# Optimization experiments

Hardware: AMD Instinct MI355X
Metric: run time of the kernel (lower is better)

The kernel has to match this reference:

```python
import jax, jax.numpy as jnp
import numpy as np

B, T, C = 2, 2048, 1024
NH = 16
HD = C // NH

def setup_inputs() -> dict:
    key = jax.random.key(0)
    ks = jax.random.split(key, 4)
    x = jax.random.normal(ks[0], (B, T, C), dtype=jnp.float32)
    w_attn = jax.random.normal(ks[1], (C, 3 * C), dtype=jnp.float32) * (1.0 / np.sqrt(C))
    b_attn = jnp.zeros((3 * C,), dtype=jnp.float32)
    w_proj = jax.random.normal(ks[2], (C, C), dtype=jnp.float32) * (1.0 / np.sqrt(C))
    b_proj = jnp.zeros((C,), dtype=jnp.float32)
    return {"x": x, "w_attn": w_attn, "b_attn": b_attn, "w_proj": w_proj, "b_proj": b_proj}

def reference(x, w_attn, b_attn, w_proj, b_proj):
    Bq, Tq, Cq = x.shape
    qkv = x @ w_attn + b_attn                      # [B,T,3C]
    q, k, v = jnp.split(qkv, 3, axis=2)
    # [B,T,C] -> [B,NH,T,HD]
    def heads(t):
        return t.reshape(Bq, Tq, NH, HD).transpose(0, 2, 1, 3)
    q, k, v = heads(q), heads(k), heads(v)
    att = jnp.einsum('bhqd,bhkd->bhqk', q, k) * (1.0 / np.sqrt(HD))
    causal = jnp.tril(jnp.ones((Tq, Tq), dtype=bool))
    att = jnp.where(causal[None, None], att, -jnp.inf)
    att = jax.nn.softmax(att, axis=-1)
    y = jnp.einsum('bhqk,bhkd->bhqd', att, v)      # [B,NH,T,HD]
    y = y.transpose(0, 2, 1, 3).reshape(Bq, Tq, Cq)
    return y @ w_proj + b_proj
```

## Files before the change

kernel.cpp:

```cpp
#include <hip/hip_runtime.h>

typedef unsigned short u16;
typedef short bf16x8 __attribute__((ext_vector_type(8)));
typedef float f32x4 __attribute__((ext_vector_type(4)));

#define BATCH 2
#define SEQ   2048
#define CH    1024
#define NHEAD 16
#define HDIM  64
#define ROWS  (BATCH*SEQ)

#define SWZ(r_, c_) (((r_)*64) + ((c_) ^ (((r_)&7)*8)))

__device__ __forceinline__ u16 f2b(float f) {
  unsigned u = __builtin_bit_cast(unsigned, f);
  u += 0x7FFFu + ((u >> 16) & 1u);
  return (u16)(u >> 16);
}
__device__ __forceinline__ float b2f(u16 h) {
  unsigned u = ((unsigned)h) << 16;
  return __builtin_bit_cast(float, u);
}
__device__ __forceinline__ float exp2_fast(float x) {
  float r; asm("v_exp_f32 %0, %1" : "=v"(r) : "v"(x)); return r;
}
__device__ __forceinline__ unsigned cvt_pk_bf16(float a, float b) {
  unsigned r; asm("v_cvt_pk_bf16_f32 %0, %1, %2" : "=v"(r) : "v"(a), "v"(b)); return r;
}

__device__ __forceinline__ void gload_lds16(const void* g, void* l) {
  __builtin_amdgcn_global_load_lds(
      (const __attribute__((address_space(1))) unsigned int*)g,
      (__attribute__((address_space(3))) unsigned int*)l, 16, 0, 0);
}

__global__ void csa_convert_x(const float* __restrict__ in, u16* __restrict__ out,
                              int n8) {
  int i = blockIdx.x * 256 + threadIdx.x;
  if (i >= n8) return;
  const float4* f4 = (const float4*)in;
  float4 v0 = f4[2*i], v1 = f4[2*i+1];
  ushort4 o0, o1;
  o0.x = f2b(v0.x); o0.y = f2b(v0.y); o0.z = f2b(v0.z); o0.w = f2b(v0.w);
  o1.x = f2b(v1.x); o1.y = f2b(v1.y); o1.z = f2b(v1.z); o1.w = f2b(v1.w);
  ((ushort4*)out)[2*i]   = o0;
  ((ushort4*)out)[2*i+1] = o1;
}

__global__ void csa_transpose2(const float* __restrict__ wa, const float* __restrict__ wp,
                               u16* __restrict__ wat, u16* __restrict__ wpt) {
  __shared__ float tile[32][33];
  int bx = blockIdx.x;
  const float* in; u16* out; int C;
  if (bx < 96) { in = wa; out = wat; C = 3*CH; }
  else         { in = wp; out = wpt; C = CH; bx -= 96; }
  const int R = CH;
  const int bxc = bx * 32, by = blockIdx.y * 32;
  const int tx = threadIdx.x, ty = threadIdx.y;
  #pragma unroll
  for (int j = 0; j < 4; ++j) {
    int r = by + ty + j*8, c = bxc + tx;
    tile[ty + j*8][tx] = in[(size_t)r*C + c];
  }
  __syncthreads();
  #pragma unroll
  for (int j = 0; j < 4; ++j) {
    int oc = bxc + ty + j*8;
    int orr = by + tx;
    out[(size_t)oc*R + orr] = f2b(tile[tx][ty + j*8]);
  }
}

__global__ __launch_bounds__(512) void csa_gemm_qkv(
    const u16* __restrict__ A, const u16* __restrict__ Bt,
    const float* __restrict__ bias,
    u16* __restrict__ qbo, u16* __restrict__ kb, u16* __restrict__ vtb)
{
  __shared__ __align__(16) u16 As[2][256*64];
  __shared__ __align__(16) u16 Bs[2][192*64];
  const int t = threadIdx.x, lane = t & 63, w = t >> 6;
  const int wm = w >> 2, wn = w & 3, g = lane >> 4, qi = lane & 15;

  const int wgid = blockIdx.y * 16 + blockIdx.x;
  const int c8 = wgid & 7, inner = wgid >> 3;
  const int bm = (c8 >> 1) * 4 + (inner >> 3);
  const int bn = (c8 & 1) * 8 + (inner & 7);

  f32x4 acc[8][3] = {};

  const u16* Ab = A  + (size_t)(bm*256)*CH;
  const u16* Bb = Bt + (size_t)(bn*192)*CH;
  const int srow = t >> 3;
  const int scol = (t & 7) * 8;

  #pragma unroll
  for (int p = 0; p < 4; ++p)
    gload_lds16(Ab + (size_t)(p*64 + srow)*CH + scol, &As[0][p*4096 + w*512]);
  #pragma unroll
  for (int p = 0; p < 3; ++p)
    gload_lds16(Bb + (size_t)(p*64 + srow)*CH + scol, &Bs[0][p*4096 + w*512]);
  __syncthreads();

  int cur = 0;
  for (int k0 = 0; k0 < CH; k0 += 64) {
    if (k0 + 64 < CH) {
      #pragma unroll
      for (int p = 0; p < 4; ++p)
        gload_lds16(Ab + (size_t)(p*64 + srow)*CH + (k0+64) + scol, &As[cur^1][p*4096 + w*512]);
      #pragma unroll
      for (int p = 0; p < 3; ++p)
        gload_lds16(Bb + (size_t)(p*64 + srow)*CH + (k0+64) + scol, &Bs[cur^1][p*4096 + w*512]);
    }
    #pragma unroll
    for (int kk = 0; kk < 2; ++kk) {
      bf16x8 af[8], bfr[3];
      #pragma unroll
      for (int m = 0; m < 8; ++m)
        af[m] = *(const bf16x8*)&As[cur][(wm*128 + m*16 + qi)*64 + kk*32 + g*8];
      #pragma unroll
      for (int n = 0; n < 3; ++n)
        bfr[n] = *(const bf16x8*)&Bs[cur][(wn*48 + n*16 + qi)*64 + kk*32 + g*8];
      #pragma unroll
      for (int m = 0; m < 8; ++m)
        #pragma unroll
        for (int n = 0; n < 3; ++n)
          acc[m][n] = __builtin_amdgcn_mfma_f32_16x16x32_bf16(af[m], bfr[n], acc[m][n], 0, 0, 0);
    }
    __syncthreads();
    cur ^= 1;
  }

  #pragma unroll
  for (int m = 0; m < 8; ++m) {
    const int row0 = bm*256 + wm*128 + m*16 + g*4;
    const int bb = row0 >> 11;
    const int t0 = row0 & 2047;
    #pragma unroll
    for (int n = 0; n < 3; ++n) {
      const int col = bn*192 + wn*48 + n*16 + qi;
      const float bv = bias[col];
      const int which = col >> 10;
      const int cc = col & 1023;
      const int h = cc >> 6, d = cc & 63;
      const int bh = bb*16 + h;
      if (which == 2) {
        ushort4 pw;
        pw.x = f2b(acc[m][n][0] + bv);
        pw.y = f2b(acc[m][n][1] + bv);
        pw.z = f2b(acc[m][n][2] + bv);
        pw.w = f2b(acc[m][n][3] + bv);
        *(ushort4*)&vtb[((size_t)bh*HDIM + d)*SEQ + t0] = pw;
      } else {
        u16* dst = (which == 0) ? qbo : kb;
        #pragma unroll
        for (int r = 0; r < 4; ++r)
          dst[((size_t)bh*SEQ + t0 + r)*HDIM + d] = f2b(acc[m][n][r] + bv);
      }
    }
  }
}

__global__ __launch_bounds__(256) void csa_gemm_proj(
    const u16* __restrict__ A, const u16* __restrict__ Bt,
    const float* __restrict__ bias, float* __restrict__ out)
{
  __shared__ __align__(16) u16 As[2][128*64];
  __shared__ __align__(16) u16 Bs[2][128*64];
  const int t = threadIdx.x, lane = t & 63, w = t >> 6;
  const int wm = w >> 1, wn = w & 1, g = lane >> 4, qi = lane & 15;
  const int bm = blockIdx.y, bn = blockIdx.x;

  f32x4 acc[4][4] = {};

  const u16* Ab = A  + (size_t)(bm*128)*CH;
  const u16* Bb = Bt + (size_t)(bn*128)*CH;
  const int srow = t >> 3;
  const int scol = (t & 7) * 8;

  #pragma unroll
  for (int p = 0; p < 4; ++p) {
    gload_lds16(Ab + (size_t)(p*32 + srow)*CH + scol, &As[0][p*2048 + w*512]);
    gload_lds16(Bb + (size_t)(p*32 + srow)*CH + scol, &Bs[0][p*2048 + w*512]);
  }
  __syncthreads();

  int cur = 0;
  for (int k0 = 0; k0 < CH; k0 += 64) {
    if (k0 + 64 < CH) {
      #pragma unroll
      for (int p = 0; p < 4; ++p) {
        gload_lds16(Ab + (size_t)(p*32 + srow)*CH + (k0+64) + scol, &As[cur^1][p*2048 + w*512]);
        gload_lds16(Bb + (size_t)(p*32 + srow)*CH + (k0+64) + scol, &Bs[cur^1][p*2048 + w*512]);
      }
    }
    #pragma unroll
    for (int kk = 0; kk < 2; ++kk) {
      bf16x8 af[4], bfr[4];
      #pragma unroll
      for (int m = 0; m < 4; ++m)
        af[m] = *(const bf16x8*)&As[cur][(wm*64 + m*16 + qi)*64 + kk*32 + g*8];
      #pragma unroll
      for (int n = 0; n < 4; ++n)
        bfr[n] = *(const bf16x8*)&Bs[cur][(wn*64 + n*16 + qi)*64 + kk*32 + g*8];
      #pragma unroll
      for (int m = 0; m < 4; ++m)
        #pragma unroll
        for (int n = 0; n < 4; ++n)
          acc[m][n] = __builtin_amdgcn_mfma_f32_16x16x32_bf16(af[m], bfr[n], acc[m][n], 0, 0, 0);
    }
    __syncthreads();
    cur ^= 1;
  }

  #pragma unroll
  for (int m = 0; m < 4; ++m) {
    const int row0 = bm*128 + wm*64 + m*16 + g*4;
    #pragma unroll
    for (int n = 0; n < 4; ++n) {
      const int col = bn*128 + wn*64 + n*16 + qi;
      const float bv = bias[col];
      #pragma unroll
      for (int r = 0; r < 4; ++r)
        out[(size_t)(row0 + r)*CH + col] = acc[m][n][r] + bv;
    }
  }
}

__global__ __launch_bounds__(512) void csa_attn(
    const u16* __restrict__ qb, const u16* __restrict__ kb,
    const u16* __restrict__ vtb, u16* __restrict__ yout)
{
  const int bh = blockIdx.x, pair = blockIdx.y;
  const int bidx = bh >> 4, h = bh & 15;
  const int t = threadIdx.x, lane = t & 63, w = t >> 6;
  const int g = lane >> 4, qi = lane & 15;
  __shared__ __align__(16) u16 Ks[2][64*64];
  __shared__ __align__(16) u16 Vs[2][64*64];
  __shared__ __align__(16) u16 Ps[8][16*64];

  const size_t kvbase = (size_t)bh * SEQ * HDIM;
  const int srow = t >> 3;
  const int ssw  = (srow & 7) * 8;
  const int scol = ((t & 7) * 8) ^ ssw;

  int offK[2][4], offPw[4], offPr[2];
  #pragma unroll
  for (int c = 0; c < 2; ++c) {
    offPr[c] = SWZ(qi, c*32 + g*8);
    #pragma unroll
    for (int s4 = 0; s4 < 4; ++s4) offK[c][s4] = SWZ(s4*16 + qi, c*32 + g*8);
  }
  #pragma unroll
  for (int s4 = 0; s4 < 4; ++s4) offPw[s4] = SWZ(qi, s4*16 + g*4);

  const float QSCALE = 0.18033688011112042f;

  for (int half = 0; half < 2; ++half) {
    const int qt = half ? (15 - pair) : pair;
    const int qrow = qt*128 + w*16;
    const int nkt = 2*qt + 2;
    const int kend = qrow >> 6;

    bf16x8 qf[2];
    #pragma unroll
    for (int c = 0; c < 2; ++c) {
      qf[c] = *(const bf16x8*)&qb[(kvbase + (size_t)(qrow + qi)*HDIM) + c*32 + g*8];
      #pragma unroll
      for (int e = 0; e < 8; ++e)
        qf[c][e] = (short)f2b(b2f((u16)qf[c][e]) * QSCALE);
    }

    f32x4 yacc[4] = {};
    float mrun = -1e30f, srun = 0.f;

    gload_lds16(kb  + kvbase + (size_t)srow*HDIM + scol, &Ks[0][w*512]);
    gload_lds16(vtb + kvbase + (size_t)srow*SEQ  + scol, &Vs[0][w*512]);
    __syncthreads();

    int cur = 0;
    for (int kt = 0; kt < nkt; ++kt) {
      if (kt + 1 < nkt) {
        const int k1 = (kt + 1) * 64;
        gload_lds16(kb  + kvbase + (size_t)(k1 + srow)*HDIM + scol, &Ks[cur^1][w*512]);
        gload_lds16(vtb + kvbase + (size_t)srow*SEQ + k1 + scol,    &Vs[cur^1][w*512]);
      }

      if (kt <= kend) {
        f32x4 st[4] = {};
        #pragma unroll
        for (int c = 0; c < 2; ++c)
          #pragma unroll
          for (int s4 = 0; s4 < 4; ++s4) {
            bf16x8 kf = *(const bf16x8*)&Ks[cur][offK[c][s4]];
            st[s4] = __builtin_amdgcn_mfma_f32_16x16x32_bf16(kf, qf[c], st[s4], 0, 0, 0);
          }

        if (kt == kend) {
          const int lq = (qrow & 63) + qi;
          #pragma unroll
          for (int s4 = 0; s4 < 4; ++s4)
            #pragma unroll
            for (int r = 0; r < 4; ++r)
              if (s4*16 + g*4 + r > lq) st[s4][r] = -3.0e38f;
        }

        float tmax = st[0][0];
        #pragma unroll
        for (int s4 = 0; s4 < 4; ++s4)
          #pragma unroll
          for (int r = 0; r < 4; ++r) tmax = fmaxf(tmax, st[s4][r]);
        tmax = fmaxf(tmax, __shfl_xor(tmax, 16));
        tmax = fmaxf(tmax, __shfl_xor(tmax, 32));
        if (!__all(tmax - mrun <= 11.5f)) {
          float mnew = fmaxf(mrun, tmax);
          float fac = exp2_fast(mrun - mnew);
          #pragma unroll
          for (int r = 0; r < 4; ++r) {
            float fr = __shfl(fac, g*4 + r);
            #pragma unroll
            for (int nf = 0; nf < 4; ++nf) yacc[nf][r] *= fr;
          }
          srun *= fac;
          mrun = mnew;
        }
        float tsum = 0.f;
        #pragma unroll
        for (int s4 = 0; s4 < 4; ++s4)
          #pragma unroll
          for (int r = 0; r < 4; ++r) {
            float pv = exp2_fast(st[s4][r] - mrun);
            st[s4][r] = pv;
            tsum += pv;
          }
        tsum += __shfl_xor(tsum, 16);
        tsum += __shfl_xor(tsum, 32);
        srun += tsum;

        #pragma unroll
        for (int s4 = 0; s4 < 4; ++s4) {
          uint2 pw;
          pw.x = cvt_pk_bf16(st[s4][0], st[s4][1]);
          pw.y = cvt_pk_bf16(st[s4][2], st[s4][3]);
          *(uint2*)&Ps[w][offPw[s4]] = pw;
        }

        #pragma unroll
        for (int c = 0; c < 2; ++c) {
          bf16x8 pa = *(const bf16x8*)&Ps[w][offPr[c]];
          #pragma unroll
          for (int nf = 0; nf < 4; ++nf) {
            bf16x8 vf = *(const bf16x8*)&Vs[cur][offK[c][nf]];
            yacc[nf] = __builtin_amdgcn_mfma_f32_16x16x32_bf16(pa, vf, yacc[nf], 0, 0, 0);
          }
        }
      }

      __syncthreads();
      cur ^= 1;
    }

    #pragma unroll
    for (int r = 0; r < 4; ++r) {
      float sv = __shfl(srun, g*4 + r);
      float inv = 1.f / sv;
      int qg = qrow + g*4 + r;
      #pragma unroll
      for (int nf = 0; nf < 4; ++nf) {
        int d = nf*16 + qi;
        yout[((size_t)bidx*SEQ + qg)*CH + h*HDIM + d] = f2b(yacc[nf][r] * inv);
      }
    }
  }
}

extern "C" void kernel_launch(void* const* d_in, const int* in_sizes, int n_in,
                              void* d_out, int out_size, void* d_ws, size_t ws_size,
                              hipStream_t stream) {
  (void)in_sizes; (void)n_in; (void)out_size; (void)ws_size;
  const float* x      = (const float*)d_in[0];
  const float* w_attn = (const float*)d_in[1];
  const float* b_attn = (const float*)d_in[2];
  const float* w_proj = (const float*)d_in[3];
  const float* b_proj = (const float*)d_in[4];

  char* ws = (char*)d_ws;
  const size_t MB = 1024*1024;
  u16* xb  = (u16*)(ws);
  u16* wat = (u16*)(ws +  8*MB);
  u16* wpt = (u16*)(ws + 14*MB);
  u16* qb  = (u16*)(ws + 16*MB);
  u16* kb  = (u16*)(ws + 24*MB);
  u16* vtb = (u16*)(ws + 32*MB);

  csa_convert_x<<<2048, 256, 0, stream>>>(x, xb, ROWS*CH/8);
  csa_transpose2<<<dim3(128, 32), dim3(32, 8), 0, stream>>>(w_attn, w_proj, wat, wpt);
  csa_gemm_qkv<<<dim3(16, 16), 512, 0, stream>>>(xb, wat, b_attn, qb, kb, vtb);
  csa_attn<<<dim3(32, 8), 512, 0, stream>>>(qb, kb, vtb, xb);
  csa_gemm_proj<<<dim3(8, 32), 256, 0, stream>>>(xb, wpt, b_proj, (float*)d_out);
}
```

Before: 119.7 us.

## Software-pipeline QK^T of next KV tile with softmax and PV of current tile

Restructures the attention loop so the QK^T MFMAs for tile kt+1 run while softmax and PV for tile kt are processed. K stays double-buffered and V becomes triple-buffered, with loads issued two tiles ahead and one barrier per iteration at the top of the loop. Cross-lane shuffles for the row max now run only when a rescale is needed, and the row-sum reduction is deferred to the epilogue. It also raises wave priority around the PV MFMAs. In exchange it uses more registers and LDS, which may reduce occupancy.

```diff
diff --git a/kernel.cpp b/kernel.cpp
--- a/kernel.cpp
+++ b/kernel.cpp
@@ -236,7 +236,7 @@
   const int t = threadIdx.x, lane = t & 63, w = t >> 6;
   const int g = lane >> 4, qi = lane & 15;
   __shared__ __align__(16) u16 Ks[2][64*64];
-  __shared__ __align__(16) u16 Vs[2][64*64];
+  __shared__ __align__(16) u16 Vs[3][64*64];
   __shared__ __align__(16) u16 Ps[8][16*64];
 
   const size_t kvbase = (size_t)bh * SEQ * HDIM;
@@ -277,25 +277,42 @@
     gload_lds16(kb  + kvbase + (size_t)srow*HDIM + scol, &Ks[0][w*512]);
     gload_lds16(vtb + kvbase + (size_t)srow*SEQ  + scol, &Vs[0][w*512]);
     __syncthreads();
-
-    int cur = 0;
+    if (nkt > 1) {
+      gload_lds16(kb  + kvbase + (size_t)(64 + srow)*HDIM + scol, &Ks[1][w*512]);
+      gload_lds16(vtb + kvbase + (size_t)srow*SEQ + 64 + scol,    &Vs[1][w*512]);
+    }
+    f32x4 st[4] = {};
+    #pragma unroll
+    for (int c = 0; c < 2; ++c)
+      #pragma unroll
+      for (int s4 = 0; s4 < 4; ++s4) {
+        bf16x8 kf = *(const bf16x8*)&Ks[0][offK[c][s4]];
+        st[s4] = __builtin_amdgcn_mfma_f32_16x16x32_bf16(kf, qf[c], st[s4], 0, 0, 0);
+      }
+
+    int v0i = 0, v2i = 2;
     for (int kt = 0; kt < nkt; ++kt) {
-      if (kt + 1 < nkt) {
-        const int k1 = (kt + 1) * 64;
-        gload_lds16(kb  + kvbase + (size_t)(k1 + srow)*HDIM + scol, &Ks[cur^1][w*512]);
-        gload_lds16(vtb + kvbase + (size_t)srow*SEQ + k1 + scol,    &Vs[cur^1][w*512]);
-      }
-
-      if (kt <= kend) {
-        f32x4 st[4] = {};
+      __syncthreads();
+
+      if (kt + 2 < nkt) {
+        const int k2 = (kt + 2) * 64;
+        gload_lds16(kb  + kvbase + (size_t)(k2 + srow)*HDIM + scol, &Ks[kt & 1][w*512]);
+        gload_lds16(vtb + kvbase + (size_t)srow*SEQ + k2 + scol,    &Vs[v2i][w*512]);
+      }
+
+      f32x4 st2[4] = {};
+      const bool doqk = (kt + 1 <= kend);
+      if (doqk) {
         #pragma unroll
         for (int c = 0; c < 2; ++c)
           #pragma unroll
           for (int s4 = 0; s4 < 4; ++s4) {
-            bf16x8 kf = *(const bf16x8*)&Ks[cur][offK[c][s4]];
-            st[s4] = __builtin_amdgcn_mfma_f32_16x16x32_bf16(kf, qf[c], st[s4], 0, 0, 0);
+            bf16x8 kf = *(const bf16x8*)&Ks[(kt + 1) & 1][offK[c][s4]];
+            st2[s4] = __builtin_amdgcn_mfma_f32_16x16x32_bf16(kf, qf[c], st2[s4], 0, 0, 0);
           }
-
+      }
+
+      if (kt <= kend) {
         if (kt == kend) {
           const int lq = (qrow & 63) + qi;
           #pragma unroll
@@ -305,15 +322,16 @@
               if (s4*16 + g*4 + r > lq) st[s4][r] = -3.0e38f;
         }
 
-        float tmax = st[0][0];
-        #pragma unroll
-        for (int s4 = 0; s4 < 4; ++s4)
-          #pragma unroll
-          for (int r = 0; r < 4; ++r) tmax = fmaxf(tmax, st[s4][r]);
-        tmax = fmaxf(tmax, __shfl_xor(tmax, 16));
-        tmax = fmaxf(tmax, __shfl_xor(tmax, 32));
+        float m0 = fmaxf(fmaxf(fmaxf(st[0][0], st[0][1]), st[0][2]), st[0][3]);
+        float m1 = fmaxf(fmaxf(fmaxf(st[1][0], st[1][1]), st[1][2]), st[1][3]);
+        float m2 = fmaxf(fmaxf(fmaxf(st[2][0], st[2][1]), st[2][2]), st[2][3]);
+        float m3 = fmaxf(fmaxf(fmaxf(st[3][0], st[3][1]), st[3][2]), st[3][3]);
+        float tmax = fmaxf(fmaxf(fmaxf(m0, m1), m2), m3);
+
         if (!__all(tmax - mrun <= 11.5f)) {
-          float mnew = fmaxf(mrun, tmax);
+          float tmf = fmaxf(tmax, __shfl_xor(tmax, 16));
+          tmf = fmaxf(tmf, __shfl_xor(tmf, 32));
+          float mnew = fmaxf(mrun, tmf);
           float fac = exp2_fast(mrun - mnew);
           #pragma unroll
           for (int r = 0; r < 4; ++r) {
@@ -333,8 +351,6 @@
             st[s4][r] = pv;
             tsum += pv;
           }
-        tsum += __shfl_xor(tsum, 16);
-        tsum += __shfl_xor(tsum, 32);
         srun += tsum;
 
         #pragma unroll
@@ -345,24 +361,32 @@
           *(uint2*)&Ps[w][offPw[s4]] = pw;
         }
 
+        __builtin_amdgcn_s_setprio(1);
         #pragma unroll
         for (int c = 0; c < 2; ++c) {
           bf16x8 pa = *(const bf16x8*)&Ps[w][offPr[c]];
           #pragma unroll
           for (int nf = 0; nf < 4; ++nf) {
-            bf16x8 vf = *(const bf16x8*)&Vs[cur][offK[c][nf]];
+            bf16x8 vf = *(const bf16x8*)&Vs[v0i][offK[c][nf]];
             yacc[nf] = __builtin_amdgcn_mfma_f32_16x16x32_bf16(pa, vf, yacc[nf], 0, 0, 0);
           }
         }
-      }
-
-      __syncthreads();
-      cur ^= 1;
-    }
-
+        __builtin_amdgcn_s_setprio(0);
+      }
+
+      if (doqk) {
+        #pragma unroll
+        for (int s4 = 0; s4 < 4; ++s4) st[s4] = st2[s4];
+      }
+      v0i = (v0i == 2) ? 0 : v0i + 1;
+      v2i = (v2i == 2) ? 0 : v2i + 1;
+    }
+
+    float srf = srun + __shfl_xor(srun, 16);
+    srf += __shfl_xor(srf, 32);
     #pragma unroll
     for (int r = 0; r < 4; ++r) {
-      float sv = __shfl(srun, g*4 + r);
+      float sv = __shfl(srf, g*4 + r);
       float inv = 1.f / sv;
       int qg = qrow + g*4 + r;
       #pragma unroll
```

Result: no change. 119.4 us (-0.2%).
